# Kernel optimization log

Hardware: AMD Instinct MI355X
Metric: run time of the kernel (lower is better)

## Reference

```python
import jax, jax.numpy as jnp
import numpy as np

# Irrep layout of node_vec: 128x0e | 64x1e (64*3) | 32x2e (32*5)
MUL0, MUL1, MUL2 = 128, 64, 32
A = 32  # node_attr scalar channels (32x0e)
N = 8192


def setup_inputs() -> dict:
    key = jax.random.key(0)
    ks = jax.random.split(key, 12)
    f32 = jnp.float32
    return {
        "node_vec": jax.random.normal(ks[0], (N, MUL0 + 3 * MUL1 + 5 * MUL2), f32),
        "node_embedding": jax.random.normal(ks[1], (N, A), f32),
        # fctp_1: TP(input, attr) -> gated irreps (scalars + gates + vectors)
        "W1s": jax.random.normal(ks[2], (MUL0, A, MUL0), f32),          # 0e x 0e -> 0e
        "b1s": jnp.zeros((MUL0,), f32),
        "W1g": jax.random.normal(ks[3], (MUL0, A, MUL1 + MUL2), f32),   # 0e x 0e -> gate 0e
        "b1g": jnp.zeros((MUL1 + MUL2,), f32),
        "W1v1": jax.random.normal(ks[4], (MUL1, A, MUL1), f32),         # 1e x 0e -> 1e
        "W1v2": jax.random.normal(ks[5], (MUL2, A, MUL2), f32),         # 2e x 0e -> 2e
        # fctp_2: TP(mlp_mid, attr) -> 32x0e (only scalar path allowed by CG rules)
        "W2": jax.random.normal(ks[6], (MUL0, A, A), f32),
        "b2": jnp.zeros((A,), f32),
        # output network: LinearRS(32->32) + SiLU + LinearRS(32->1)
        "W3": jax.random.normal(ks[7], (A, A), f32),
        "b3": jnp.zeros((A,), f32),
        "W4": jax.random.normal(ks[8], (A, 1), f32),
        "b4": jnp.zeros((1,), f32),
    }


def reference(node_vec, node_embedding, W1s, b1s, W1g, b1g, W1v1, W1v2, W2, b2, W3, b3, W4, b4):
    n = node_vec.shape[0]
    attr = node_embedding
    # split features by irrep degree
    s = node_vec[:, :MUL0]                                         # [n,128]   0e
    v1 = node_vec[:, MUL0:MUL0 + 3 * MUL1].reshape(n, MUL1, 3)     # [n,64,3]  1e
    v2 = node_vec[:, MUL0 + 3 * MUL1:].reshape(n, MUL2, 5)         # [n,32,5]  2e

    inv = lambda u: 1.0 / np.sqrt(u * A).astype(np.float32)

    # ---- fctp_1: fully-connected TP with scalar attr (l x 0e -> l per-path mixing) ----
    s_mid = jnp.einsum('nu,nv,uvw->nw', s, attr, W1s) * inv(MUL0) + b1s
    g = jnp.einsum('nu,nv,uvw->nw', s, attr, W1g) * inv(MUL0) + b1g
    v1_mid = jnp.einsum('num,nv,uvw->nwm', v1, attr, W1v1) * inv(MUL1)
    v2_mid = jnp.einsum('num,nv,uvw->nwm', v2, attr, W1v2) * inv(MUL2)

    # ---- SwishGate: SiLU on scalars, sigmoid gates on vectors ----
    s_act = jax.nn.silu(s_mid)
    gate = jax.nn.sigmoid(g)
    v1_g = v1_mid * gate[:, :MUL1, None]
    v2_g = v2_mid * gate[:, MUL1:, None]
    # NOTE: v1_g/v2_g have no allowed CG path into the 0e output of fctp_2 (l x 0 -> 0
    # only for l=0), so they do not contribute — exactly as in the original module.
    del v1_g, v2_g

    # ---- fctp_2: mlp_mid x attr -> 32x0e (scalar path only) ----
    h = jnp.einsum('nu,nv,uvw->nw', s_act, attr, W2) * inv(MUL0) + b2

    # ---- output network: LinearRS + SiLU + LinearRS ----
    h = jax.nn.silu(h @ (W3 / np.sqrt(A).astype(np.float32)) + b3)
    pred_energy = h @ (W4 / np.sqrt(A).astype(np.float32)) + b4     # [n,1]
    return pred_energy
```

## Files before the change

kernel.cpp:

```cpp
#include <hip/hip_runtime.h>

typedef _Float16 f16;
typedef f16 f16x8 __attribute__((ext_vector_type(8)));
typedef f16 f16x4 __attribute__((ext_vector_type(4)));
typedef f16 f16x2 __attribute__((ext_vector_type(2)));
typedef float f32x4 __attribute__((ext_vector_type(4)));

union F8 { uint4 u4; f16x8 v; f16x2 h[4]; f16 e[8]; };

__global__ __launch_bounds__(256) void prep_kernel(
    const float* __restrict__ W1s, const float* __restrict__ W2,
    f16* __restrict__ W1P, f16* __restrict__ W2P)
{
    __shared__ f16 T[32 * 36];
    const int b = blockIdx.x, t = threadIdx.x;

    const float* src; f16* dst; int u, w0, W;
    if (b < 512) { u = b >> 2; w0 = (b & 3) * 32; W = 128; src = W1s; dst = W1P; }
    else         { u = b - 512; w0 = 0;           W = 32;  src = W2;  dst = W2P; }
    {
        int v = t >> 3, wq = t & 7;
        float4 f = *(const float4*)(src + (size_t)(u * 32 + v) * W + w0 + wq * 4);
        T[v * 36 + wq * 4 + 0] = (f16)f.x;
        T[v * 36 + wq * 4 + 1] = (f16)f.y;
        T[v * 36 + wq * 4 + 2] = (f16)f.z;
        T[v * 36 + wq * 4 + 3] = (f16)f.w;
    }
    __syncthreads();
    {
        int w = t >> 3, vr = t & 7;
        f16x4 o = { T[(vr * 4 + 0) * 36 + w], T[(vr * 4 + 1) * 36 + w],
                    T[(vr * 4 + 2) * 36 + w], T[(vr * 4 + 3) * 36 + w] };
        *(f16x4*)(dst + (size_t)u * (W * 32) + (size_t)(w0 + w) * 32 + vr * 4) = o;
    }
}

__global__ __launch_bounds__(512, 2) void fused_kernel(
    const float* __restrict__ node_vec, const float* __restrict__ attr,
    const f16* __restrict__ W1P, const float* __restrict__ b1s,
    const f16* __restrict__ W2P, const float* __restrict__ b2,
    const float* __restrict__ W3, const float* __restrict__ b3,
    const float* __restrict__ W4, const float* __restrict__ b4,
    float* __restrict__ out)
{
    __shared__ alignas(16) f16   s_lds[32 * 136];
    __shared__ alignas(16) f16   sact_lds[32 * 136];
    __shared__ alignas(16) float red[8][32 * 36];
    __shared__ alignas(16) float W3_lds[32 * 36];
    __shared__ alignas(16) float h_lds[32 * 36];

    const int t  = threadIdx.x;
    const int n0 = blockIdx.x * 32;
    const int wv = t >> 6, l = t & 63, lr = l & 15, q = l >> 4;
    const int c0 = wv * 16;
    const int u0 = wv * 16;

    #pragma unroll
    for (int i = 0; i < 2; ++i) {
        int idx = t + 512 * i;
        int r = idx >> 5, c4 = idx & 31;
        float4 f = *(const float4*)(node_vec + (size_t)(n0 + r) * 480 + c4 * 4);
        f16x4 o = { (f16)f.x, (f16)f.y, (f16)f.z, (f16)f.w };
        *(f16x4*)(s_lds + r * 136 + c4 * 4) = o;
    }
    if (t < 256) {
        int i = t >> 3, jj = (t & 7) * 4;
        *(f32x4*)(W3_lds + i * 36 + jj) = *(const f32x4*)(W3 + i * 32 + jj);
    }

    F8 af0, af1;
    #pragma unroll
    for (int kk = 0; kk < 4; ++kk) {
        float2 fa = *(const float2*)(attr + (size_t)(n0 + lr) * 32 + q * 8 + kk * 2);
        float2 fb = *(const float2*)(attr + (size_t)(n0 + 16 + lr) * 32 + q * 8 + kk * 2);
        af0.h[kk] = f16x2{ (f16)fa.x, (f16)fa.y };
        af1.h[kk] = f16x2{ (f16)fb.x, (f16)fb.y };
    }

    const f16* Bp = W1P + ((size_t)(c0 + lr)) * 32 + q * 8;
    f16x8 B[8];
    #pragma unroll
    for (int j = 0; j < 8; ++j)
        B[j] = *(const f16x8*)(Bp + (size_t)j * 4096);

    __syncthreads();

    f32x4 acc0 = {0.f, 0.f, 0.f, 0.f}, acc1 = {0.f, 0.f, 0.f, 0.f};

    F8 s8[2][2];
    s8[0][0].v = *(const f16x8*)(s_lds + lr * 136);
    s8[0][1].v = *(const f16x8*)(s_lds + (16 + lr) * 136);

    #pragma unroll
    for (int uo = 0; uo < 16; ++uo) {
        const int cur = uo & 1, nxt = cur ^ 1;
        const int uon = (uo + 1 < 16) ? uo + 1 : 15;
        s8[nxt][0].v = *(const f16x8*)(s_lds + lr * 136 + uon * 8);
        s8[nxt][1].v = *(const f16x8*)(s_lds + (16 + lr) * 136 + uon * 8);
        #pragma unroll
        for (int j = 0; j < 8; ++j) {
            const int u = uo * 8 + j;
            f16x8 bf = B[j];
            if (u + 8 < 128)
                B[j] = *(const f16x8*)(Bp + (size_t)(u + 8) * 4096);
            f16 sv0 = s8[cur][0].e[j];
            f16 sv1 = s8[cur][1].e[j];
            f16x2 sb0 = { sv0, sv0 }, sb1 = { sv1, sv1 };
            F8 a0, a1;
            #pragma unroll
            for (int kk = 0; kk < 4; ++kk) {
                a0.h[kk] = sb0 * af0.h[kk];
                a1.h[kk] = sb1 * af1.h[kk];
            }
            acc0 = __builtin_amdgcn_mfma_f32_16x16x32_f16(a0.v, bf, acc0, 0, 0, 0);
            acc1 = __builtin_amdgcn_mfma_f32_16x16x32_f16(a1.v, bf, acc1, 0, 0, 0);
        }
    }

    {
        const float bv = b1s[c0 + lr];
        #pragma unroll
        for (int reg = 0; reg < 4; ++reg) {
            float v0 = acc0[reg] * 0.015625f + bv;
            float v1 = acc1[reg] * 0.015625f + bv;
            sact_lds[(q * 4 + reg) * 136 + c0 + lr]        = (f16)(v0 / (1.f + __expf(-v0)));
            sact_lds[(16 + q * 4 + reg) * 136 + c0 + lr]   = (f16)(v1 / (1.f + __expf(-v1)));
        }
    }

    const f16* B2p = W2P + ((size_t)u0 * 32 + lr) * 32 + q * 8;
    f16x8 B0[8], B1[8];
    #pragma unroll
    for (int j = 0; j < 8; ++j) {
        B0[j] = *(const f16x8*)(B2p + (size_t)j * 1024);
        B1[j] = *(const f16x8*)(B2p + (size_t)j * 1024 + 512);
    }

    __syncthreads();

    f32x4 acc00 = {0,0,0,0}, acc01 = {0,0,0,0};
    f32x4 acc10 = {0,0,0,0}, acc11 = {0,0,0,0};

    F8 t8[2][2];
    t8[0][0].v = *(const f16x8*)(sact_lds + lr * 136 + u0);
    t8[0][1].v = *(const f16x8*)(sact_lds + (16 + lr) * 136 + u0);

    #pragma unroll
    for (int uo = 0; uo < 2; ++uo) {
        const int cur = uo & 1, nxt = cur ^ 1;
        const int uon = (uo + 1 < 2) ? uo + 1 : 1;
        t8[nxt][0].v = *(const f16x8*)(sact_lds + lr * 136 + u0 + uon * 8);
        t8[nxt][1].v = *(const f16x8*)(sact_lds + (16 + lr) * 136 + u0 + uon * 8);
        #pragma unroll
        for (int j = 0; j < 8; ++j) {
            const int k = uo * 8 + j;
            f16x8 bf0 = B0[j], bf1 = B1[j];
            if (k + 8 < 16) {
                B0[j] = *(const f16x8*)(B2p + (size_t)(k + 8) * 1024);
                B1[j] = *(const f16x8*)(B2p + (size_t)(k + 8) * 1024 + 512);
            }
            f16 sv0 = t8[cur][0].e[j];
            f16 sv1 = t8[cur][1].e[j];
            f16x2 sb0 = { sv0, sv0 }, sb1 = { sv1, sv1 };
            F8 a0, a1;
            #pragma unroll
            for (int kk = 0; kk < 4; ++kk) {
                a0.h[kk] = sb0 * af0.h[kk];
                a1.h[kk] = sb1 * af1.h[kk];
            }
            acc00 = __builtin_amdgcn_mfma_f32_16x16x32_f16(a0.v, bf0, acc00, 0, 0, 0);
            acc01 = __builtin_amdgcn_mfma_f32_16x16x32_f16(a0.v, bf1, acc01, 0, 0, 0);
            acc10 = __builtin_amdgcn_mfma_f32_16x16x32_f16(a1.v, bf0, acc10, 0, 0, 0);
            acc11 = __builtin_amdgcn_mfma_f32_16x16x32_f16(a1.v, bf1, acc11, 0, 0, 0);
        }
    }

    #pragma unroll
    for (int reg = 0; reg < 4; ++reg) {
        red[wv][(q * 4 + reg) * 36 + lr]           = acc00[reg];
        red[wv][(q * 4 + reg) * 36 + 16 + lr]      = acc01[reg];
        red[wv][(16 + q * 4 + reg) * 36 + lr]      = acc10[reg];
        red[wv][(16 + q * 4 + reg) * 36 + 16 + lr] = acc11[reg];
    }
    __syncthreads();

    {
        int row = t >> 4, c2 = (t & 15) * 2;
        float s0 = 0.f, s1 = 0.f;
        #pragma unroll
        for (int w = 0; w < 8; ++w) {
            s0 += red[w][row * 36 + c2];
            s1 += red[w][row * 36 + c2 + 1];
        }
        h_lds[row * 36 + c2]     = s0 * 0.015625f + b2[c2];
        h_lds[row * 36 + c2 + 1] = s1 * 0.015625f + b2[c2 + 1];
    }
    __syncthreads();

    {
        int node = t >> 4, jj = (t & 15) * 2;
        float a0 = 0.f, a1 = 0.f;
        #pragma unroll
        for (int i = 0; i < 32; ++i) {
            float hv = h_lds[node * 36 + i];
            a0 += hv * W3_lds[i * 36 + jj];
            a1 += hv * W3_lds[i * 36 + jj + 1];
        }
        const float inv = 0.17677669529663687f;
        float p = 0.f;
        float aa[2] = { a0, a1 };
        #pragma unroll
        for (int e = 0; e < 2; ++e) {
            float tv = aa[e] * inv + b3[jj + e];
            float g  = tv / (1.f + __expf(-tv));
            p += g * W4[jj + e] * inv;
        }
        p += __shfl_xor(p, 1);
        p += __shfl_xor(p, 2);
        p += __shfl_xor(p, 4);
        p += __shfl_xor(p, 8);
        if ((t & 15) == 0) out[n0 + node] = p + b4[0];
    }
}

extern "C" void kernel_launch(void* const* d_in, const int* in_sizes, int n_in,
                              void* d_out, int out_size, void* d_ws, size_t ws_size,
                              hipStream_t stream)
{
    const float* node_vec = (const float*)d_in[0];
    const float* attr     = (const float*)d_in[1];
    const float* W1s      = (const float*)d_in[2];
    const float* b1s      = (const float*)d_in[3];
    const float* W2       = (const float*)d_in[8];
    const float* b2       = (const float*)d_in[9];
    const float* W3       = (const float*)d_in[10];
    const float* b3       = (const float*)d_in[11];
    const float* W4       = (const float*)d_in[12];
    const float* b4       = (const float*)d_in[13];
    float* out = (float*)d_out;

    char* ws = (char*)d_ws;
    f16* W1P = (f16*)(ws);
    f16* W2P = (f16*)(ws + (1u << 20));

    prep_kernel<<<640, 256, 0, stream>>>(W1s, W2, W1P, W2P);
    fused_kernel<<<256, 512, 0, stream>>>(node_vec, attr, W1P, b1s,
                                          W2P, b2, W3, b3, W4, b4, out);
}
```

Baseline: 109.7 us.

## Fuse weight prep into main kernel using cooperative grid sync

Removes the separate prep kernel launch. The fused kernel now converts and transposes W1s/W2 into fp16 packed layouts itself, with each half-block handling one or two transpose tiles. A cooperative-groups grid barrier replaces the kernel boundary, and the launch becomes hipLaunchCooperativeKernel. This saves one launch and its gap, at the cost of a grid-wide sync, extra LDS for the transpose tiles, and the requirement that all 256 blocks are co-resident.

Measured after the change: 213.5 us. 1.95x slower.

```diff
diff --git a/kernel.cpp b/kernel.cpp
--- a/kernel.cpp
+++ b/kernel.cpp
@@ -1,4 +1,7 @@
 #include <hip/hip_runtime.h>
+#include <hip/hip_cooperative_groups.h>
+
+namespace cg = cooperative_groups;
 
 typedef _Float16 f16;
 typedef f16 f16x8 __attribute__((ext_vector_type(8)));
@@ -8,39 +11,13 @@
 
 union F8 { uint4 u4; f16x8 v; f16x2 h[4]; f16 e[8]; };
 
-__global__ __launch_bounds__(256) void prep_kernel(
-    const float* __restrict__ W1s, const float* __restrict__ W2,
-    f16* __restrict__ W1P, f16* __restrict__ W2P)
-{
-    __shared__ f16 T[32 * 36];
-    const int b = blockIdx.x, t = threadIdx.x;
-
-    const float* src; f16* dst; int u, w0, W;
-    if (b < 512) { u = b >> 2; w0 = (b & 3) * 32; W = 128; src = W1s; dst = W1P; }
-    else         { u = b - 512; w0 = 0;           W = 32;  src = W2;  dst = W2P; }
-    {
-        int v = t >> 3, wq = t & 7;
-        float4 f = *(const float4*)(src + (size_t)(u * 32 + v) * W + w0 + wq * 4);
-        T[v * 36 + wq * 4 + 0] = (f16)f.x;
-        T[v * 36 + wq * 4 + 1] = (f16)f.y;
-        T[v * 36 + wq * 4 + 2] = (f16)f.z;
-        T[v * 36 + wq * 4 + 3] = (f16)f.w;
-    }
-    __syncthreads();
-    {
-        int w = t >> 3, vr = t & 7;
-        f16x4 o = { T[(vr * 4 + 0) * 36 + w], T[(vr * 4 + 1) * 36 + w],
-                    T[(vr * 4 + 2) * 36 + w], T[(vr * 4 + 3) * 36 + w] };
-        *(f16x4*)(dst + (size_t)u * (W * 32) + (size_t)(w0 + w) * 32 + vr * 4) = o;
-    }
-}
-
 __global__ __launch_bounds__(512, 2) void fused_kernel(
     const float* __restrict__ node_vec, const float* __restrict__ attr,
-    const f16* __restrict__ W1P, const float* __restrict__ b1s,
-    const f16* __restrict__ W2P, const float* __restrict__ b2,
-    const float* __restrict__ W3, const float* __restrict__ b3,
-    const float* __restrict__ W4, const float* __restrict__ b4,
+    const float* __restrict__ W1s, const float* __restrict__ b1s,
+    const float* __restrict__ W2,  const float* __restrict__ b2,
+    const float* __restrict__ W3,  const float* __restrict__ b3,
+    const float* __restrict__ W4,  const float* __restrict__ b4,
+    f16* __restrict__ W1P, f16* __restrict__ W2P,
     float* __restrict__ out)
 {
     __shared__ alignas(16) f16   s_lds[32 * 136];
@@ -48,12 +25,44 @@
     __shared__ alignas(16) float red[8][32 * 36];
     __shared__ alignas(16) float W3_lds[32 * 36];
     __shared__ alignas(16) float h_lds[32 * 36];
+    __shared__ alignas(16) f16   T[2][32 * 36];
 
     const int t  = threadIdx.x;
     const int n0 = blockIdx.x * 32;
     const int wv = t >> 6, l = t & 63, lr = l & 15, q = l >> 4;
     const int c0 = wv * 16;
     const int u0 = wv * 16;
+
+    {
+        const int grp = (blockIdx.x << 1) | (t >> 8);
+        const int tt  = t & 255;
+        f16* Tb = T[t >> 8];
+        #pragma unroll
+        for (int pass = 0; pass < 2; ++pass) {
+            const int vb = grp + pass * 512;
+            if (vb < 640) {
+                const float* src; f16* dst; int u, w0, W;
+                if (vb < 512) { u = vb >> 2; w0 = (vb & 3) * 32; W = 128; src = W1s; dst = W1P; }
+                else          { u = vb - 512; w0 = 0;            W = 32;  src = W2;  dst = W2P; }
+                {
+                    int v = tt >> 3, wq = tt & 7;
+                    float4 f = *(const float4*)(src + (size_t)(u * 32 + v) * W + w0 + wq * 4);
+                    Tb[v * 36 + wq * 4 + 0] = (f16)f.x;
+                    Tb[v * 36 + wq * 4 + 1] = (f16)f.y;
+                    Tb[v * 36 + wq * 4 + 2] = (f16)f.z;
+                    Tb[v * 36 + wq * 4 + 3] = (f16)f.w;
+                }
+                __syncthreads();
+                {
+                    int w = tt >> 3, vr = tt & 7;
+                    f16x4 o = { Tb[(vr * 4 + 0) * 36 + w], Tb[(vr * 4 + 1) * 36 + w],
+                                Tb[(vr * 4 + 2) * 36 + w], Tb[(vr * 4 + 3) * 36 + w] };
+                    *(f16x4*)(dst + (size_t)u * (W * 32) + (size_t)(w0 + w) * 32 + vr * 4) = o;
+                }
+                __syncthreads();
+            }
+        }
+    }
 
     #pragma unroll
     for (int i = 0; i < 2; ++i) {
@@ -67,7 +76,6 @@
         int i = t >> 3, jj = (t & 7) * 4;
         *(f32x4*)(W3_lds + i * 36 + jj) = *(const f32x4*)(W3 + i * 32 + jj);
     }
-
     F8 af0, af1;
     #pragma unroll
     for (int kk = 0; kk < 4; ++kk) {
@@ -77,13 +85,14 @@
         af1.h[kk] = f16x2{ (f16)fb.x, (f16)fb.y };
     }
 
+    __threadfence();
+    cg::this_grid().sync();
+
     const f16* Bp = W1P + ((size_t)(c0 + lr)) * 32 + q * 8;
     f16x8 B[8];
     #pragma unroll
     for (int j = 0; j < 8; ++j)
         B[j] = *(const f16x8*)(Bp + (size_t)j * 4096);
-
-    __syncthreads();
 
     f32x4 acc0 = {0.f, 0.f, 0.f, 0.f}, acc1 = {0.f, 0.f, 0.f, 0.f};
 
@@ -123,8 +132,8 @@
         for (int reg = 0; reg < 4; ++reg) {
             float v0 = acc0[reg] * 0.015625f + bv;
             float v1 = acc1[reg] * 0.015625f + bv;
-            sact_lds[(q * 4 + reg) * 136 + c0 + lr]        = (f16)(v0 / (1.f + __expf(-v0)));
-            sact_lds[(16 + q * 4 + reg) * 136 + c0 + lr]   = (f16)(v1 / (1.f + __expf(-v1)));
+            sact_lds[(q * 4 + reg) * 136 + c0 + lr]      = (f16)(v0 / (1.f + __expf(-v0)));
+            sact_lds[(16 + q * 4 + reg) * 136 + c0 + lr] = (f16)(v1 / (1.f + __expf(-v1)));
         }
     }
 
@@ -243,7 +252,11 @@
     f16* W1P = (f16*)(ws);
     f16* W2P = (f16*)(ws + (1u << 20));
 
-    prep_kernel<<<640, 256, 0, stream>>>(W1s, W2, W1P, W2P);
-    fused_kernel<<<256, 512, 0, stream>>>(node_vec, attr, W1P, b1s,
-                                          W2P, b2, W3, b3, W4, b4, out);
+    void* args[] = {
+        (void*)&node_vec, (void*)&attr, (void*)&W1s, (void*)&b1s,
+        (void*)&W2, (void*)&b2, (void*)&W3, (void*)&b3,
+        (void*)&W4, (void*)&b4, (void*)&W1P, (void*)&W2P, (void*)&out
+    };
+    hipLaunchCooperativeKernel((const void*)fused_kernel,
+                               dim3(256), dim3(512), args, 0, stream);
 }
```

## Tile fused TP kernel as 64 rows by half-width columns with cross-block reduction

Applied to the files above, without the earlier changes.

Each block now handles 64 nodes and half of the 128 output channels of the first tensor product, with the input dimension split across two wave groups and reduced through LDS. This reuses each W1 fragment across four row tiles instead of two, roughly halving total W1 traffic from L2. The second-stage partial results for the two column halves go to a global buffer. The last-arriving block of each pair, found with an atomic counter whose flags are cleared in the prep kernel, finishes the output MLP. This adds global round-trips, atomics and fences, and relies on correct memory ordering between blocks.

Measured after the change: 131.6 us. 1.2x slower.

```diff
diff --git a/kernel.cpp b/kernel.cpp
--- a/kernel.cpp
+++ b/kernel.cpp
@@ -10,10 +10,13 @@
 
 __global__ __launch_bounds__(256) void prep_kernel(
     const float* __restrict__ W1s, const float* __restrict__ W2,
-    f16* __restrict__ W1P, f16* __restrict__ W2P)
+    f16* __restrict__ W1P, f16* __restrict__ W2P,
+    unsigned int* __restrict__ flags)
 {
     __shared__ f16 T[32 * 36];
     const int b = blockIdx.x, t = threadIdx.x;
+
+    if (b == 639 && t < 128) flags[t] = 0u;
 
     const float* src; f16* dst; int u, w0, W;
     if (b < 512) { u = b >> 2; w0 = (b & 3) * 32; W = 128; src = W1s; dst = W1P; }
@@ -41,22 +44,36 @@
     const f16* __restrict__ W2P, const float* __restrict__ b2,
     const float* __restrict__ W3, const float* __restrict__ b3,
     const float* __restrict__ W4, const float* __restrict__ b4,
+    float* __restrict__ hbuf, unsigned int* __restrict__ flags,
     float* __restrict__ out)
 {
-    __shared__ alignas(16) f16   s_lds[32 * 136];
-    __shared__ alignas(16) f16   sact_lds[32 * 136];
-    __shared__ alignas(16) float red[8][32 * 36];
+    __shared__ alignas(16) f16   s_lds[64 * 136];
+    __shared__ alignas(16) f16   sact_lds[64 * 72];
+    __shared__ alignas(16) float redbuf[4096];
     __shared__ alignas(16) float W3_lds[32 * 36];
-    __shared__ alignas(16) float h_lds[32 * 36];
-
-    const int t  = threadIdx.x;
-    const int n0 = blockIdx.x * 32;
+    __shared__ alignas(16) float h_lds[64 * 36];
+    __shared__ int flag_sh;
+
+    const int t   = threadIdx.x;
+    const int bid = blockIdx.x;
+    const int cg = (bid >> 3) & 1;
+    const int rg = (bid & 7) * 16 + (bid >> 4);
+    const int n0 = rg * 64;
+    const int wbase = cg * 64;
+
     const int wv = t >> 6, l = t & 63, lr = l & 15, q = l >> 4;
-    const int c0 = wv * 16;
-    const int u0 = wv * 16;
-
-    #pragma unroll
-    for (int i = 0; i < 2; ++i) {
+    const int s1 = wv & 3, h1 = wv >> 2;
+    const int rt2 = wv >> 1, us2 = wv & 1;
+
+    const f16* Bp = W1P + (size_t)(h1 * 64) * 4096
+                        + (size_t)(wbase + s1 * 16 + lr) * 32 + q * 8;
+    f16x8 B[8];
+    #pragma unroll
+    for (int j = 0; j < 8; ++j)
+        B[j] = *(const f16x8*)(Bp + (size_t)j * 4096);
+
+    #pragma unroll
+    for (int i = 0; i < 4; ++i) {
         int idx = t + 512 * i;
         int r = idx >> 5, c4 = idx & 31;
         float4 f = *(const float4*)(node_vec + (size_t)(n0 + r) * 480 + c4 * 4);
@@ -68,158 +85,177 @@
         *(f32x4*)(W3_lds + i * 36 + jj) = *(const f32x4*)(W3 + i * 32 + jj);
     }
 
-    F8 af0, af1;
-    #pragma unroll
-    for (int kk = 0; kk < 4; ++kk) {
-        float2 fa = *(const float2*)(attr + (size_t)(n0 + lr) * 32 + q * 8 + kk * 2);
-        float2 fb = *(const float2*)(attr + (size_t)(n0 + 16 + lr) * 32 + q * 8 + kk * 2);
-        af0.h[kk] = f16x2{ (f16)fa.x, (f16)fa.y };
-        af1.h[kk] = f16x2{ (f16)fb.x, (f16)fb.y };
-    }
-
-    const f16* Bp = W1P + ((size_t)(c0 + lr)) * 32 + q * 8;
-    f16x8 B[8];
-    #pragma unroll
-    for (int j = 0; j < 8; ++j)
-        B[j] = *(const f16x8*)(Bp + (size_t)j * 4096);
-
-    __syncthreads();
-
-    f32x4 acc0 = {0.f, 0.f, 0.f, 0.f}, acc1 = {0.f, 0.f, 0.f, 0.f};
-
-    F8 s8[2][2];
-    s8[0][0].v = *(const f16x8*)(s_lds + lr * 136);
-    s8[0][1].v = *(const f16x8*)(s_lds + (16 + lr) * 136);
-
-    #pragma unroll
-    for (int uo = 0; uo < 16; ++uo) {
+    F8 af[4];
+    #pragma unroll
+    for (int rt = 0; rt < 4; ++rt) {
+        #pragma unroll
+        for (int kk = 0; kk < 4; ++kk) {
+            float2 fa = *(const float2*)(attr + (size_t)(n0 + rt * 16 + lr) * 32 + q * 8 + kk * 2);
+            af[rt].h[kk] = f16x2{ (f16)fa.x, (f16)fa.y };
+        }
+    }
+
+    __syncthreads();
+
+    f32x4 acc[4] = { {0,0,0,0}, {0,0,0,0}, {0,0,0,0}, {0,0,0,0} };
+
+    F8 s8[2][4];
+    #pragma unroll
+    for (int rt = 0; rt < 4; ++rt)
+        s8[0][rt].v = *(const f16x8*)(s_lds + (rt * 16 + lr) * 136 + h1 * 64);
+
+    #pragma unroll
+    for (int uo = 0; uo < 8; ++uo) {
         const int cur = uo & 1, nxt = cur ^ 1;
-        const int uon = (uo + 1 < 16) ? uo + 1 : 15;
-        s8[nxt][0].v = *(const f16x8*)(s_lds + lr * 136 + uon * 8);
-        s8[nxt][1].v = *(const f16x8*)(s_lds + (16 + lr) * 136 + uon * 8);
+        const int uon = (uo + 1 < 8) ? uo + 1 : 7;
+        #pragma unroll
+        for (int rt = 0; rt < 4; ++rt)
+            s8[nxt][rt].v = *(const f16x8*)(s_lds + (rt * 16 + lr) * 136 + h1 * 64 + uon * 8);
         #pragma unroll
         for (int j = 0; j < 8; ++j) {
-            const int u = uo * 8 + j;
             f16x8 bf = B[j];
-            if (u + 8 < 128)
-                B[j] = *(const f16x8*)(Bp + (size_t)(u + 8) * 4096);
-            f16 sv0 = s8[cur][0].e[j];
-            f16 sv1 = s8[cur][1].e[j];
-            f16x2 sb0 = { sv0, sv0 }, sb1 = { sv1, sv1 };
-            F8 a0, a1;
-            #pragma unroll
-            for (int kk = 0; kk < 4; ++kk) {
-                a0.h[kk] = sb0 * af0.h[kk];
-                a1.h[kk] = sb1 * af1.h[kk];
-            }
-            acc0 = __builtin_amdgcn_mfma_f32_16x16x32_f16(a0.v, bf, acc0, 0, 0, 0);
-            acc1 = __builtin_amdgcn_mfma_f32_16x16x32_f16(a1.v, bf, acc1, 0, 0, 0);
-        }
-    }
-
-    {
-        const float bv = b1s[c0 + lr];
-        #pragma unroll
-        for (int reg = 0; reg < 4; ++reg) {
-            float v0 = acc0[reg] * 0.015625f + bv;
-            float v1 = acc1[reg] * 0.015625f + bv;
-            sact_lds[(q * 4 + reg) * 136 + c0 + lr]        = (f16)(v0 / (1.f + __expf(-v0)));
-            sact_lds[(16 + q * 4 + reg) * 136 + c0 + lr]   = (f16)(v1 / (1.f + __expf(-v1)));
-        }
-    }
-
-    const f16* B2p = W2P + ((size_t)u0 * 32 + lr) * 32 + q * 8;
+            if (uo * 8 + j + 8 < 64)
+                B[j] = *(const f16x8*)(Bp + (size_t)(uo * 8 + j + 8) * 4096);
+            #pragma unroll
+            for (int rt = 0; rt < 4; ++rt) {
+                f16 sv = s8[cur][rt].e[j];
+                f16x2 sb = { sv, sv };
+                F8 a;
+                #pragma unroll
+                for (int kk = 0; kk < 4; ++kk)
+                    a.h[kk] = sb * af[rt].h[kk];
+                acc[rt] = __builtin_amdgcn_mfma_f32_16x16x32_f16(a.v, bf, acc[rt], 0, 0, 0);
+            }
+        }
+    }
+
+    const f16* B2p = W2P + (size_t)(wbase + us2 * 32) * 1024 + (size_t)lr * 32 + q * 8;
     f16x8 B0[8], B1[8];
     #pragma unroll
     for (int j = 0; j < 8; ++j) {
         B0[j] = *(const f16x8*)(B2p + (size_t)j * 1024);
         B1[j] = *(const f16x8*)(B2p + (size_t)j * 1024 + 512);
     }
-
-    __syncthreads();
-
-    f32x4 acc00 = {0,0,0,0}, acc01 = {0,0,0,0};
-    f32x4 acc10 = {0,0,0,0}, acc11 = {0,0,0,0};
-
-    F8 t8[2][2];
-    t8[0][0].v = *(const f16x8*)(sact_lds + lr * 136 + u0);
-    t8[0][1].v = *(const f16x8*)(sact_lds + (16 + lr) * 136 + u0);
-
-    #pragma unroll
-    for (int uo = 0; uo < 2; ++uo) {
+    F8 af2;
+    #pragma unroll
+    for (int kk = 0; kk < 4; ++kk) {
+        float2 fa = *(const float2*)(attr + (size_t)(n0 + rt2 * 16 + lr) * 32 + q * 8 + kk * 2);
+        af2.h[kk] = f16x2{ (f16)fa.x, (f16)fa.y };
+    }
+
+    if (h1 == 0) {
+        #pragma unroll
+        for (int rt = 0; rt < 4; ++rt)
+            #pragma unroll
+            for (int reg = 0; reg < 4; ++reg)
+                redbuf[s1 * 1024 + (rt * 16 + q * 4 + reg) * 16 + lr] = acc[rt][reg];
+    }
+    __syncthreads();
+    if (h1 == 1) {
+        const float bv = b1s[wbase + s1 * 16 + lr];
+        #pragma unroll
+        for (int rt = 0; rt < 4; ++rt) {
+            #pragma unroll
+            for (int reg = 0; reg < 4; ++reg) {
+                float v0 = acc[rt][reg]
+                         + redbuf[s1 * 1024 + (rt * 16 + q * 4 + reg) * 16 + lr];
+                v0 = v0 * 0.015625f + bv;
+                sact_lds[(rt * 16 + q * 4 + reg) * 72 + s1 * 16 + lr] =
+                    (f16)(v0 / (1.f + __expf(-v0)));
+            }
+        }
+    }
+    __syncthreads();
+
+    f32x4 acc20 = {0,0,0,0}, acc21 = {0,0,0,0};
+
+    F8 t8[2];
+    t8[0].v = *(const f16x8*)(sact_lds + (rt2 * 16 + lr) * 72 + us2 * 32);
+
+    #pragma unroll
+    for (int uo = 0; uo < 4; ++uo) {
         const int cur = uo & 1, nxt = cur ^ 1;
-        const int uon = (uo + 1 < 2) ? uo + 1 : 1;
-        t8[nxt][0].v = *(const f16x8*)(sact_lds + lr * 136 + u0 + uon * 8);
-        t8[nxt][1].v = *(const f16x8*)(sact_lds + (16 + lr) * 136 + u0 + uon * 8);
+        const int uon = (uo + 1 < 4) ? uo + 1 : 3;
+        t8[nxt].v = *(const f16x8*)(sact_lds + (rt2 * 16 + lr) * 72 + us2 * 32 + uon * 8);
         #pragma unroll
         for (int j = 0; j < 8; ++j) {
-            const int k = uo * 8 + j;
             f16x8 bf0 = B0[j], bf1 = B1[j];
-            if (k + 8 < 16) {
-                B0[j] = *(const f16x8*)(B2p + (size_t)(k + 8) * 1024);
-                B1[j] = *(const f16x8*)(B2p + (size_t)(k + 8) * 1024 + 512);
-            }
-            f16 sv0 = t8[cur][0].e[j];
-            f16 sv1 = t8[cur][1].e[j];
-            f16x2 sb0 = { sv0, sv0 }, sb1 = { sv1, sv1 };
-            F8 a0, a1;
-            #pragma unroll
-            for (int kk = 0; kk < 4; ++kk) {
-                a0.h[kk] = sb0 * af0.h[kk];
-                a1.h[kk] = sb1 * af1.h[kk];
-            }
-            acc00 = __builtin_amdgcn_mfma_f32_16x16x32_f16(a0.v, bf0, acc00, 0, 0, 0);
-            acc01 = __builtin_amdgcn_mfma_f32_16x16x32_f16(a0.v, bf1, acc01, 0, 0, 0);
-            acc10 = __builtin_amdgcn_mfma_f32_16x16x32_f16(a1.v, bf0, acc10, 0, 0, 0);
-            acc11 = __builtin_amdgcn_mfma_f32_16x16x32_f16(a1.v, bf1, acc11, 0, 0, 0);
-        }
-    }
-
-    #pragma unroll
-    for (int reg = 0; reg < 4; ++reg) {
-        red[wv][(q * 4 + reg) * 36 + lr]           = acc00[reg];
-        red[wv][(q * 4 + reg) * 36 + 16 + lr]      = acc01[reg];
-        red[wv][(16 + q * 4 + reg) * 36 + lr]      = acc10[reg];
-        red[wv][(16 + q * 4 + reg) * 36 + 16 + lr] = acc11[reg];
-    }
-    __syncthreads();
-
-    {
-        int row = t >> 4, c2 = (t & 15) * 2;
-        float s0 = 0.f, s1 = 0.f;
-        #pragma unroll
-        for (int w = 0; w < 8; ++w) {
-            s0 += red[w][row * 36 + c2];
-            s1 += red[w][row * 36 + c2 + 1];
-        }
-        h_lds[row * 36 + c2]     = s0 * 0.015625f + b2[c2];
-        h_lds[row * 36 + c2 + 1] = s1 * 0.015625f + b2[c2 + 1];
-    }
-    __syncthreads();
-
-    {
-        int node = t >> 4, jj = (t & 15) * 2;
-        float a0 = 0.f, a1 = 0.f;
-        #pragma unroll
-        for (int i = 0; i < 32; ++i) {
-            float hv = h_lds[node * 36 + i];
-            a0 += hv * W3_lds[i * 36 + jj];
-            a1 += hv * W3_lds[i * 36 + jj + 1];
-        }
-        const float inv = 0.17677669529663687f;
-        float p = 0.f;
-        float aa[2] = { a0, a1 };
-        #pragma unroll
-        for (int e = 0; e < 2; ++e) {
-            float tv = aa[e] * inv + b3[jj + e];
-            float g  = tv / (1.f + __expf(-tv));
-            p += g * W4[jj + e] * inv;
-        }
-        p += __shfl_xor(p, 1);
-        p += __shfl_xor(p, 2);
-        p += __shfl_xor(p, 4);
-        p += __shfl_xor(p, 8);
-        if ((t & 15) == 0) out[n0 + node] = p + b4[0];
+            if (uo * 8 + j + 8 < 32) {
+                B0[j] = *(const f16x8*)(B2p + (size_t)(uo * 8 + j + 8) * 1024);
+                B1[j] = *(const f16x8*)(B2p + (size_t)(uo * 8 + j + 8) * 1024 + 512);
+            }
+            f16 sv = t8[cur].e[j];
+            f16x2 sb = { sv, sv };
+            F8 a;
+            #pragma unroll
+            for (int kk = 0; kk < 4; ++kk)
+                a.h[kk] = sb * af2.h[kk];
+            acc20 = __builtin_amdgcn_mfma_f32_16x16x32_f16(a.v, bf0, acc20, 0, 0, 0);
+            acc21 = __builtin_amdgcn_mfma_f32_16x16x32_f16(a.v, bf1, acc21, 0, 0, 0);
+        }
+    }
+
+    if (us2 == 1) {
+        #pragma unroll
+        for (int reg = 0; reg < 4; ++reg) {
+            redbuf[rt2 * 512 + (q * 4 + reg) * 32 + lr]      = acc20[reg];
+            redbuf[rt2 * 512 + (q * 4 + reg) * 32 + 16 + lr] = acc21[reg];
+        }
+    }
+    __syncthreads();
+    if (us2 == 0) {
+        #pragma unroll
+        for (int reg = 0; reg < 4; ++reg) {
+            float c0v = acc20[reg] + redbuf[rt2 * 512 + (q * 4 + reg) * 32 + lr];
+            float c1v = acc21[reg] + redbuf[rt2 * 512 + (q * 4 + reg) * 32 + 16 + lr];
+            size_t row = (size_t)(n0 + rt2 * 16 + q * 4 + reg);
+            hbuf[((size_t)cg * 8192 + row) * 32 + lr]      = c0v;
+            hbuf[((size_t)cg * 8192 + row) * 32 + 16 + lr] = c1v;
+        }
+    }
+    __syncthreads();
+
+    if (t == 0) {
+        __threadfence();
+        flag_sh = (int)atomicAdd(&flags[rg], 1u);
+    }
+    __syncthreads();
+    if (flag_sh == 1) {
+        __threadfence();
+        {
+            int r = t >> 3, j4 = (t & 7) * 4;
+            f32x4 a = *(const f32x4*)(hbuf + ((size_t)0 * 8192 + n0 + r) * 32 + j4);
+            f32x4 b = *(const f32x4*)(hbuf + ((size_t)1 * 8192 + n0 + r) * 32 + j4);
+            #pragma unroll
+            for (int e = 0; e < 4; ++e)
+                h_lds[r * 36 + j4 + e] = (a[e] + b[e]) * 0.015625f + b2[j4 + e];
+        }
+        __syncthreads();
+        {
+            int node = t >> 3, j4 = (t & 7) * 4;
+            float a0 = 0.f, a1 = 0.f, a2 = 0.f, a3 = 0.f;
+            #pragma unroll
+            for (int i = 0; i < 32; ++i) {
+                float hv = h_lds[node * 36 + i];
+                a0 += hv * W3_lds[i * 36 + j4 + 0];
+                a1 += hv * W3_lds[i * 36 + j4 + 1];
+                a2 += hv * W3_lds[i * 36 + j4 + 2];
+                a3 += hv * W3_lds[i * 36 + j4 + 3];
+            }
+            const float inv = 0.17677669529663687f;
+            float p = 0.f;
+            float aa[4] = { a0, a1, a2, a3 };
+            #pragma unroll
+            for (int e = 0; e < 4; ++e) {
+                float tv = aa[e] * inv + b3[j4 + e];
+                float g  = tv / (1.f + __expf(-tv));
+                p += g * W4[j4 + e] * inv;
+            }
+            p += __shfl_xor(p, 1);
+            p += __shfl_xor(p, 2);
+            p += __shfl_xor(p, 4);
+            if ((t & 7) == 0) out[n0 + node] = p + b4[0];
+        }
     }
 }
 
@@ -240,10 +276,13 @@
     float* out = (float*)d_out;
 
     char* ws = (char*)d_ws;
-    f16* W1P = (f16*)(ws);
-    f16* W2P = (f16*)(ws + (1u << 20));
-
-    prep_kernel<<<640, 256, 0, stream>>>(W1s, W2, W1P, W2P);
+    f16*   W1P   = (f16*)(ws);
+    f16*   W2P   = (f16*)(ws + (1u << 20));
+    float* hbuf  = (float*)(ws + (1280u << 10));
+    unsigned int* flags = (unsigned int*)(ws + (3328u << 10));
+
+    prep_kernel<<<640, 256, 0, stream>>>(W1s, W2, W1P, W2P, flags);
     fused_kernel<<<256, 512, 0, stream>>>(node_vec, attr, W1P, b1s,
-                                          W2P, b2, W3, b3, W4, b4, out);
+                                          W2P, b2, W3, b3, W4, b4,
+                                          hbuf, flags, out);
 }
```
